# Kernel optimization log

Hardware: AMD Instinct MI355X
Metric: run time of the kernel (lower is better)

## Reference

```python
import jax, jax.numpy as jnp
import numpy as np

LAYERS, HIDDEN, FFN, HEADS = 4, 128, 256, 4
HEAD_D = HIDDEN // HEADS          # 32
V_HEAD = 2 * HEAD_D               # 64 (double_v_dim)
V_DIM = 2 * HIDDEN                # 256
SCALE_BASE = 512
EPS = 1e-5
GAMMAS = (1.0 - np.exp(np.linspace(np.log(1.0 / 32), np.log(1.0 / 512), HEADS))).astype(np.float32)


def _xpos(x, downscale):
    # x: (..., L, d) -- xpos rotary embedding with per-position decay scale
    L, d = x.shape[-2], x.shape[-1]
    half = d // 2
    base_scale = (jnp.arange(half, dtype=jnp.float32) + 0.4 * d) / (1.4 * d)   # (half,)
    power = jnp.arange(L, dtype=jnp.float32)[:, None] / SCALE_BASE
    sc = base_scale[None, :] ** power                                          # (L, half)
    inv_freq = 1.0 / (10000.0 ** (jnp.arange(half, dtype=jnp.float32) / half))
    ang = jnp.arange(L, dtype=jnp.float32)[:, None] * inv_freq[None, :]        # (L, half)
    sin, cos = jnp.sin(ang), jnp.cos(ang)
    if downscale:
        sc = 1.0 / sc
    sin_d = jnp.repeat(sin * sc, 2, axis=-1)   # duplicate_interleave -> (L, d)
    cos_d = jnp.repeat(cos * sc, 2, axis=-1)
    x1, x2 = x[..., ::2], x[..., 1::2]
    rot = jnp.stack((-x2, x1), axis=-1).reshape(x.shape)  # rotate_every_two
    return x * cos_d + rot * sin_d


def _layer_norm(x, w, b):
    mu = x.mean(-1, keepdims=True)
    var = x.var(-1, keepdims=True)
    return (x - mu) / jnp.sqrt(var + EPS) * w + b


def _msr(X, wq, wk, wv, wg, wo, gn_w, gn_b):
    # MultiScaleRetention, parallel form. X: (B, L, HIDDEN)
    B, L, _ = X.shape
    Q = _xpos(jnp.einsum('blh,nhd->bnld', X, wq), False)   # (B, heads, L, 32)
    K = _xpos(jnp.einsum('blh,nhd->bnld', X, wk), True)
    V = jnp.einsum('blh,nhv->bnlv', X, wv)                 # (B, heads, L, 64)
    n = jnp.arange(L)
    diff = n[:, None] - n[None, :]
    gam = jnp.asarray(GAMMAS)[:, None, None]
    D = jnp.where(diff >= 0, gam ** jnp.maximum(diff, 0).astype(jnp.float32), 0.0)  # (heads, L, L)
    scores = jnp.einsum('bnld,bnmd->bnlm', Q, K) * D[None]
    Y = jnp.einsum('bnlm,bnmv->bnlv', scores, V)
    Y = Y.transpose(0, 2, 1, 3).reshape(B, L, V_DIM)       # concat heads on feature dim
    # GroupNorm(heads, V_DIM) over the channel axis
    Yg = Y.reshape(B, L, HEADS, V_HEAD)
    mu = Yg.mean(-1, keepdims=True)
    var = Yg.var(-1, keepdims=True)
    Yn = ((Yg - mu) / jnp.sqrt(var + EPS)).reshape(B, L, V_DIM) * gn_w + gn_b
    G = X @ wg
    return (G * jax.nn.sigmoid(G) * Yn) @ wo               # swish gate, output proj


def _forward(x, rem_w1, rem_b1, rem_w2, rem_b2, rem_w3, rem_b3,
             wq, wk, wv, wg, wo, gn_w, gn_b,
             ln1_w, ln1_b, ln2_w, ln2_b,
             ffn_w1, ffn_b1, ffn_w2, ffn_b2,
             dec_w1, dec_b1, dec_w2, dec_b2):
    gelu = lambda t: jax.nn.gelu(t, approximate=False)
    # REM: 5 -> 32 -> 64 -> 128, GELU after each linear
    X = gelu(gelu(gelu(x @ rem_w1 + rem_b1) @ rem_w2 + rem_b2) @ rem_w3 + rem_b3)
    # RetNet: pre-LN retention + pre-LN FFN blocks with residuals
    for i in range(LAYERS):
        Y = _msr(_layer_norm(X, ln1_w[i], ln1_b[i]), wq[i], wk[i], wv[i],
                 wg[i], wo[i], gn_w[i], gn_b[i]) + X
        Z = _layer_norm(Y, ln2_w[i], ln2_b[i])
        X = gelu(Z @ ffn_w1[i] + ffn_b1[i]) @ ffn_w2[i] + ffn_b2[i] + Y
    # Decoder: 128 -> 64 -> 20, softmax over classes
    logits = gelu(X @ dec_w1 + dec_b1) @ dec_w2 + dec_b2
    return jax.nn.softmax(logits, axis=-1)


def setup_inputs() -> dict:
    key = jax.random.key(0)
    ks = jax.random.split(key, 16)
    rn = lambda k, shape, s=0.02: jax.random.normal(k, shape, dtype=jnp.float32) * s
    B, L = 64, 512
    return {
        'x': jax.random.normal(ks[0], (B, L, 5), dtype=jnp.float32),
        'rem_w1': rn(ks[1], (5, 32)), 'rem_b1': jnp.zeros((32,), jnp.float32),
        'rem_w2': rn(ks[2], (32, 64)), 'rem_b2': jnp.zeros((64,), jnp.float32),
        'rem_w3': rn(ks[3], (64, HIDDEN)), 'rem_b3': jnp.zeros((HIDDEN,), jnp.float32),
        'wq': rn(ks[4], (LAYERS, HEADS, HIDDEN, HEAD_D), 1.0 / HIDDEN),
        'wk': rn(ks[5], (LAYERS, HEADS, HIDDEN, HEAD_D), 1.0 / HIDDEN),
        'wv': rn(ks[6], (LAYERS, HEADS, HIDDEN, V_HEAD), 1.0 / HIDDEN),
        'wg': rn(ks[7], (LAYERS, HIDDEN, V_DIM), 1.0 / HIDDEN),
        'wo': rn(ks[8], (LAYERS, V_DIM, HIDDEN), 1.0 / HIDDEN),
        'gn_w': jnp.ones((LAYERS, V_DIM), jnp.float32),
        'gn_b': jnp.zeros((LAYERS, V_DIM), jnp.float32),
        'ln1_w': jnp.ones((LAYERS, HIDDEN), jnp.float32),
        'ln1_b': jnp.zeros((LAYERS, HIDDEN), jnp.float32),
        'ln2_w': jnp.ones((LAYERS, HIDDEN), jnp.float32),
        'ln2_b': jnp.zeros((LAYERS, HIDDEN), jnp.float32),
        'ffn_w1': rn(ks[9], (LAYERS, HIDDEN, FFN)),
        'ffn_b1': jnp.zeros((LAYERS, FFN), jnp.float32),
        'ffn_w2': rn(ks[10], (LAYERS, FFN, HIDDEN)),
        'ffn_b2': jnp.zeros((LAYERS, HIDDEN), jnp.float32),
        'dec_w1': rn(ks[11], (HIDDEN, 64)), 'dec_b1': jnp.zeros((64,), jnp.float32),
        'dec_w2': rn(ks[12], (64, 20)), 'dec_b2': jnp.zeros((20,), jnp.float32),
    }


def reference(x, rem_w1, rem_b1, rem_w2, rem_b2, rem_w3, rem_b3,
              wq, wk, wv, wg, wo, gn_w, gn_b,
              ln1_w, ln1_b, ln2_w, ln2_b,
              ffn_w1, ffn_b1, ffn_w2, ffn_b2,
              dec_w1, dec_b1, dec_w2, dec_b2):
    return _forward(x, rem_w1, rem_b1, rem_w2, rem_b2, rem_w3, rem_b3,
                    wq, wk, wv, wg, wo, gn_w, gn_b,
                    ln1_w, ln1_b, ln2_w, ln2_b,
                    ffn_w1, ffn_b1, ffn_w2, ffn_b2,
                    dec_w1, dec_b1, dec_w2, dec_b2)
```

## Files before the change

kernel.cpp:

```cpp
#include <hip/hip_runtime.h>
#include <math.h>
#include <cmath>

#define SEQ   512
#define NBATCH 64
#define BT    32768
#define HID   128
#define NHEAD 4
#define HD    32
#define VHD   64
#define VDIM  256
#define FFND  256

typedef __attribute__((ext_vector_type(8))) short bf16x8;
typedef __attribute__((ext_vector_type(4))) float f32x4;
typedef unsigned short u16;

__device__ __forceinline__ float gelu_f(float x){ return 0.5f*x*(1.f+erff(x*0.70710678118f)); }

__device__ __forceinline__ u16 f2bf(float f){
  __bf16 h = (__bf16)f;
  union{__bf16 h; u16 u;} v; v.h = h; return v.u;
}
__device__ __forceinline__ float bf2f(u16 u){
  union{unsigned u; float f;} v; v.u = ((unsigned)u)<<16; return v.f;
}

__device__ __forceinline__ void gload16(const void* g, void* l){
  __builtin_amdgcn_global_load_lds(
      (const __attribute__((address_space(1))) unsigned*)g,
      (__attribute__((address_space(3))) unsigned*)l, 16, 0, 0);
}

#define STAGE_TILE_N(dst, base, strideU16, colOffU16, wid_, srow_, phys16l_, NIT) \
  do{                                                                           \
    _Pragma("unroll")                                                           \
    for(int it_=0; it_<NIT; it_++){                                             \
      int blk_ = (wid_)*NIT + it_;                                              \
      int row_ = blk_*4 + (srow_);                                              \
      int log16_ = (phys16l_) ^ (row_&15);                                      \
      gload16((base) + (size_t)row_*(strideU16) + (colOffU16) + log16_*8,       \
              &(dst)[blk_*512]);                                                \
    }                                                                           \
  }while(0)

#define STAGE_TILE(dst, base, strideU16, colOffU16, wid_, srow_, phys16l_) \
  STAGE_TILE_N(dst, base, strideU16, colOffU16, wid_, srow_, phys16l_, 8)

__global__ __launch_bounds__(256) void wconv_kernel(
    const float* __restrict__ wq, const float* __restrict__ wk,
    const float* __restrict__ wv, const float* __restrict__ wg,
    const float* __restrict__ wo, const float* __restrict__ f1,
    const float* __restrict__ f2, const float* __restrict__ dw1,
    const float* __restrict__ w2e, const float* __restrict__ w3e,
    u16* __restrict__ Wt)
{
  int idx = blockIdx.x*256 + threadIdx.x;
  if(idx >= 786432){
    int q = idx - 786432;
    if(q < 8192){ int col=q>>7, h=q&127; Wt[idx]=f2bf(dw1[h*64+col]); }
    else if(q < 10240){ int p=q-8192; int row=p>>5, col=p&31; Wt[idx]=f2bf(w2e[col*64+row]); }
    else { int p=q-10240; int row=p>>6, col=p&63; Wt[idx]=f2bf(w3e[col*128+row]); }
    return;
  }
  int layer = idx / 196608;
  int r = idx - layer*196608;
  u16* W = Wt + (size_t)layer*196608;
  const float* wq_l = wq + (size_t)layer*16384;
  const float* wk_l = wk + (size_t)layer*16384;
  const float* wv_l = wv + (size_t)layer*32768;
  const float* wg_l = wg + (size_t)layer*32768;
  const float* wo_l = wo + (size_t)layer*32768;
  const float* f1_l = f1 + (size_t)layer*32768;
  const float* f2_l = f2 + (size_t)layer*32768;
  float v;
  if(r < 98304){
    int col = r>>7, h = r&127;
    if(col<128){ int n=col>>5, d=col&31; v = wq_l[(n*128+h)*32+d]; }
    else if(col<256){ int c=col-128, n=c>>5, d=c&31; v = wk_l[(n*128+h)*32+d]; }
    else if(col<512){ int c=col-256, n=c>>6, j=c&63; v = wv_l[(n*128+h)*64+j]; }
    else { int p=col-512; v = wg_l[h*256+p]; }
    W[r] = f2bf(v);
  } else if(r < 131072){
    int q = r-98304; int col=q>>8, k=q&255;
    W[r] = f2bf(wo_l[k*128+col]);
  } else if(r < 163840){
    int q = r-131072; int col=q>>7, h=q&127;
    W[r] = f2bf(f1_l[h*256+col]);
  } else {
    int q = r-163840; int col=q>>8, k=q&255;
    W[r] = f2bf(f2_l[k*128+col]);
  }
}

__global__ __launch_bounds__(256) void embed_kernel(
    const float* __restrict__ x,
    const float* __restrict__ w1, const float* __restrict__ b1,
    const float* __restrict__ b2, const float* __restrict__ b3,
    const u16* __restrict__ W23t,
    const float* __restrict__ lnw, const float* __restrict__ lnb,
    float* __restrict__ X, u16* __restrict__ xn)
{
  __shared__ float sx[64][6];
  __shared__ float sw1[160], sb1[32], sb2[64], sb3[128];
  __shared__ u16 big[18944];
  int t=threadIdx.x, lane=t&63, wid=t>>6, mrow=lane&15, quad=lane>>4, r0=wid*16;
  int tok0=blockIdx.x*64;

  for(int i=t;i<320;i+=256) sx[i/5][i%5]=x[(size_t)tok0*5+i];
  for(int i=t;i<160;i+=256) sw1[i]=w1[i];
  if(t<32) sb1[t]=b1[t];
  if(t<64) sb2[t]=b2[t];
  if(t<128) sb3[t]=b3[t];
  for(int c=t;c<256;c+=256){ int row=c>>2, c8=(c&3)*8;
    *(uint4*)&big[2560+row*40+c8]=*(const uint4*)&W23t[row*32+c8]; }
  for(int c=t;c<1024;c+=256){ int row=c>>3, c8=(c&7)*8;
    *(uint4*)&big[9728+row*72+c8]=*(const uint4*)&W23t[2048+row*64+c8]; }
  __syncthreads();

  for(int task=t; task<2048; task+=256){
    int tok=task>>5, j=task&31;
    float a=sb1[j];
    #pragma unroll
    for(int i=0;i<5;i++) a+=sx[tok][i]*sw1[i*32+j];
    big[tok*40+j]=f2bf(gelu_f(a));
  }
  __syncthreads();

  f32x4 h2[4];
  #pragma unroll
  for(int cc=0;cc<4;cc++) h2[cc]=(f32x4){0.f,0.f,0.f,0.f};
  {
    bf16x8 a=*(const bf16x8*)&big[(r0+mrow)*40+quad*8];
    #pragma unroll
    for(int cc=0;cc<4;cc++){
      bf16x8 b=*(const bf16x8*)&big[2560+(cc*16+mrow)*40+quad*8];
      h2[cc]=__builtin_amdgcn_mfma_f32_16x16x32_bf16(a,b,h2[cc],0,0,0);
    }
  }
  #pragma unroll
  for(int cc=0;cc<4;cc++){
    float bs=sb2[cc*16+mrow];
    #pragma unroll
    for(int reg=0;reg<4;reg++)
      big[5120+(r0+quad*4+reg)*72+cc*16+mrow]=f2bf(gelu_f(h2[cc][reg]+bs));
  }
  __syncthreads();

  f32x4 xac[8];
  #pragma unroll
  for(int cc=0;cc<8;cc++) xac[cc]=(f32x4){0.f,0.f,0.f,0.f};
  #pragma unroll
  for(int ks=0;ks<2;ks++){
    bf16x8 a=*(const bf16x8*)&big[5120+(r0+mrow)*72+ks*32+quad*8];
    #pragma unroll
    for(int cc=0;cc<8;cc++){
      bf16x8 b=*(const bf16x8*)&big[9728+(cc*16+mrow)*72+ks*32+quad*8];
      xac[cc]=__builtin_amdgcn_mfma_f32_16x16x32_bf16(a,b,xac[cc],0,0,0);
    }
  }
  __syncthreads();

  #pragma unroll
  for(int reg=0;reg<4;reg++){
    int rowl=r0+quad*4+reg, rowg=tok0+rowl;
    float xv[8], s=0.f, sq=0.f;
    #pragma unroll
    for(int cc=0;cc<8;cc++){
      float v=gelu_f(xac[cc][reg]+sb3[cc*16+mrow]);
      xv[cc]=v; s+=v; sq+=v*v;
    }
    #pragma unroll
    for(int m=1;m<16;m<<=1){ s+=__shfl_xor(s,m); sq+=__shfl_xor(sq,m); }
    float mu=s*(1.f/128.f);
    float var=sq*(1.f/128.f)-mu*mu;
    float rstd=rsqrtf(var+1e-5f);
    #pragma unroll
    for(int cc=0;cc<8;cc++){
      int col=cc*16+mrow;
      X[(size_t)rowg*128+col]=xv[cc];
      big[rowl*136+col]=f2bf((xv[cc]-mu)*rstd*lnw[col]+lnb[col]);
    }
  }
  __syncthreads();
  for(int th=t; th<1024; th+=256){
    int row=th>>4, seg=th&15;
    *(uint4*)&xn[(size_t)(tok0+row)*128+seg*8]=*(const uint4*)&big[row*136+seg*8];
  }
}

__device__ __forceinline__ void qkvg_epilogue(
    int nc, f32x4 acc[2][4], u16* stg,
    int t, int mrow, int quad, int r0q, int c0q, int b, int l0, int tok0,
    u16* __restrict__ Q, u16* __restrict__ K,
    u16* __restrict__ Vt, u16* __restrict__ G)
{
  if(nc < 2){
    bool isK = (nc==1);
    float sgn = isK ? -1.f : 1.f;
    #pragma unroll
    for(int cc=0;cc<4;cc++){
      int colc = c0q + cc*16 + mrow;
      int i = (colc&31)>>1;
      float log2bs = log2f(((float)i + 12.8f)*(1.f/44.8f));
      float invf   = exp2f(-(float)i * (13.28771238f/16.f));
      float rstep  = exp2f(sgn*log2bs*(1.f/512.f));
      float c1 = cosf(invf), s1 = sinf(invf);
      #pragma unroll
      for(int rr=0;rr<2;rr++){
        int rowl0 = r0q + rr*16 + quad*4;
        float lb = (float)(l0 + rowl0);
        float sc = exp2f(sgn*log2bs*lb*(1.f/512.f));
        float ang = lb*invf;
        float u = cosf(ang)*sc, v = sinf(ang)*sc;
        #pragma unroll
        for(int reg=0;reg<4;reg++){
          int rowl = rowl0 + reg;
          float val = acc[rr][cc][reg];
          float partner = __shfl_xor(val, 1);
          float o = (colc&1) ? (val*u + partner*v) : (val*u - partner*v);
          stg[rowl*136 + colc] = f2bf(o);
          float un = (u*c1 - v*s1)*rstep;
          float vn = (u*s1 + v*c1)*rstep;
          u = un; v = vn;
        }
      }
    }
    __syncthreads();
    u16* O = isK ? K : Q;
    for(int th=t; th<1024; th+=256){
      int row=th>>4, n=(th>>2)&3, seg=th&3;
      *(uint4*)&O[(((size_t)(b*4+n)*512) + (l0+row))*32 + seg*8]
        = *(const uint4*)&stg[row*136 + n*32 + seg*8];
    }
  } else if(nc < 4){
    #pragma unroll
    for(int cc=0;cc<4;cc++){
      int colc = c0q + cc*16 + mrow;
      #pragma unroll
      for(int rr=0;rr<2;rr++){
        #pragma unroll
        for(int reg=0;reg<4;reg++){
          int rowl = r0q + rr*16 + quad*4 + reg;
          stg[colc*72 + rowl] = f2bf(acc[rr][cc][reg]);
        }
      }
    }
    __syncthreads();
    int jbase = (nc-2)*128;
    for(int th=t; th<1024; th+=256){
      int row=th>>3, seg=th&7;
      int jg = jbase + row; int n = jg>>6, j = jg&63;
      *(uint4*)&Vt[(((size_t)(b*4+n)*64) + j)*512 + l0 + seg*8]
        = *(const uint4*)&stg[row*72 + seg*8];
    }
  } else {
    #pragma unroll
    for(int cc=0;cc<4;cc++){
      int colc = c0q + cc*16 + mrow;
      #pragma unroll
      for(int rr=0;rr<2;rr++){
        #pragma unroll
        for(int reg=0;reg<4;reg++){
          int rowl = r0q + rr*16 + quad*4 + reg;
          stg[rowl*136 + colc] = f2bf(acc[rr][cc][reg]);
        }
      }
    }
    __syncthreads();
    int gc0 = (nc-4)*128;
    for(int th=t; th<1024; th+=256){
      int row=th>>4, seg=th&15;
      *(uint4*)&G[((size_t)(tok0+row))*256 + gc0 + seg*8]
        = *(const uint4*)&stg[row*136 + seg*8];
    }
  }
}

__device__ __forceinline__ void qkvg_epi8(
    int nc, f32x4 acc[4], u16* stg,
    int t, int mrow, int quad, int r0, int c0, int b, int l0, int tok0,
    u16* __restrict__ Q, u16* __restrict__ K,
    u16* __restrict__ Vt, u16* __restrict__ G)
{
  if(nc < 2){
    bool isK = (nc==1);
    float sgn = isK ? -1.f : 1.f;
    #pragma unroll
    for(int cc=0;cc<4;cc++){
      int colc = c0 + cc*16 + mrow;
      int i = (colc&31)>>1;
      float log2bs = log2f(((float)i + 12.8f)*(1.f/44.8f));
      float invf   = exp2f(-(float)i * (13.28771238f/16.f));
      float rstep  = exp2f(sgn*log2bs*(1.f/512.f));
      float c1 = cosf(invf), s1 = sinf(invf);
      int rowl0 = r0 + quad*4;
      float lb = (float)(l0 + rowl0);
      float sc = exp2f(sgn*log2bs*lb*(1.f/512.f));
      float ang = lb*invf;
      float u = cosf(ang)*sc, v = sinf(ang)*sc;
      #pragma unroll
      for(int reg=0;reg<4;reg++){
        int rowl = rowl0 + reg;
        float val = acc[cc][reg];
        float partner = __shfl_xor(val, 1);
        float o = (colc&1) ? (val*u + partner*v) : (val*u - partner*v);
        stg[rowl*136 + colc] = f2bf(o);
        float un = (u*c1 - v*s1)*rstep;
        float vn = (u*s1 + v*c1)*rstep;
        u = un; v = vn;
      }
    }
    __syncthreads();
    u16* O = isK ? K : Q;
    for(int th=t; th<1024; th+=512){
      int row=th>>4, n=(th>>2)&3, seg=th&3;
      *(uint4*)&O[(((size_t)(b*4+n)*512) + (l0+row))*32 + seg*8]
        = *(const uint4*)&stg[row*136 + n*32 + seg*8];
    }
  } else if(nc < 4){
    #pragma unroll
    for(int cc=0;cc<4;cc++){
      int colc = c0 + cc*16 + mrow;
      #pragma unroll
      for(int reg=0;reg<4;reg++){
        int rowl = r0 + quad*4 + reg;
        stg[colc*72 + rowl] = f2bf(acc[cc][reg]);
      }
    }
    __syncthreads();
    int jbase = (nc-2)*128;
    for(int th=t; th<1024; th+=512){
      int row=th>>3, seg=th&7;
      int jg = jbase + row; int n = jg>>6, j = jg&63;
      *(uint4*)&Vt[(((size_t)(b*4+n)*64) + j)*512 + l0 + seg*8]
        = *(const uint4*)&stg[row*72 + seg*8];
    }
  } else {
    #pragma unroll
    for(int cc=0;cc<4;cc++){
      int colc = c0 + cc*16 + mrow;
      #pragma unroll
      for(int reg=0;reg<4;reg++){
        int rowl = r0 + quad*4 + reg;
        stg[rowl*136 + colc] = f2bf(acc[cc][reg]);
      }
    }
    __syncthreads();
    int gc0 = (nc-4)*128;
    for(int th=t; th<1024; th+=512){
      int row=th>>4, seg=th&15;
      *(uint4*)&G[((size_t)(tok0+row))*256 + gc0 + seg*8]
        = *(const uint4*)&stg[row*136 + seg*8];
    }
  }
}

__global__ __launch_bounds__(256) void qkvg_kernel(
    const u16* __restrict__ A, const u16* __restrict__ Wt,
    u16* __restrict__ Q, u16* __restrict__ K,
    u16* __restrict__ Vt, u16* __restrict__ G)
{
  __shared__ u16 sW[128*128];
  u16* stg = sW;
  int t = threadIdx.x, lane = t&63, wid = t>>6;
  int mrow = lane&15, quad = lane>>4;
  int srow = lane>>4, phys16l = lane&15;
  int r0q = (wid>>1)*32, c0q = (wid&1)*64;
  int tok0 = blockIdx.x*64;
  int b = tok0>>9, l0 = tok0&511;

  bf16x8 a0f[4], a1f[4];
  #pragma unroll
  for(int ks=0; ks<4; ks++){
    a0f[ks] = *(const bf16x8*)&A[(size_t)(tok0+r0q+mrow)*128 + ks*32+quad*8];
    a1f[ks] = *(const bf16x8*)&A[(size_t)(tok0+r0q+16+mrow)*128 + ks*32+quad*8];
  }

  for(int ch=0; ch<3; ch++){
    int nc = blockIdx.y*3 + ch;
    if(ch) __syncthreads();
    STAGE_TILE(sW, Wt + (size_t)nc*16384, 128, 0, wid, srow, phys16l);
    __syncthreads();

    f32x4 acc[2][4];
    #pragma unroll
    for(int rr=0;rr<2;rr++)
      #pragma unroll
      for(int cc=0;cc<4;cc++) acc[rr][cc] = (f32x4){0.f,0.f,0.f,0.f};
    #pragma unroll
    for(int ks=0; ks<4; ks++){
      #pragma unroll
      for(int cc=0; cc<4; cc++){
        bf16x8 bb = *(const bf16x8*)&sW[(c0q+cc*16+mrow)*128 + (((ks*4+quad)^mrow)<<3)];
        acc[0][cc] = __builtin_amdgcn_mfma_f32_16x16x32_bf16(a0f[ks],bb,acc[0][cc],0,0,0);
        acc[1][cc] = __builtin_amdgcn_mfma_f32_16x16x32_bf16(a1f[ks],bb,acc[1][cc],0,0,0);
      }
    }
    __syncthreads();
    qkvg_epilogue(nc, acc, stg, t, mrow, quad, r0q, c0q, b, l0, tok0, Q, K, Vt, G);
  }
}

__global__ __launch_bounds__(512, 4) void layer_kernel(
    const u16* __restrict__ Qin, const u16* __restrict__ Kin,
    const u16* __restrict__ Vtin, const u16* __restrict__ Gin,
    const float* __restrict__ gnw, const float* __restrict__ gnb, float4 l2g,
    const u16* __restrict__ Wo,
    const u16* __restrict__ W1t, const float* __restrict__ b1,
    const u16* __restrict__ W2t, const float* __restrict__ b2,
    const float* __restrict__ Xin,
    const float* __restrict__ ln2w, const float* __restrict__ ln2b,
    const float* __restrict__ ln1w, const float* __restrict__ ln1b,
    float* __restrict__ Xout,
    const u16* __restrict__ Wq,
    u16* __restrict__ Qo, u16* __restrict__ Ko,
    u16* __restrict__ Vto, u16* __restrict__ Go,
    const u16* __restrict__ DecW1, const float* __restrict__ db1,
    const float* __restrict__ dw2, const float* __restrict__ db2,
    float* __restrict__ outp)
{
  __shared__ u16 smem[33280];
  u16* bufA = smem;
  u16* bufB = smem + 16384;
  float (*sRed)[2][2] = (float(*)[2][2])(smem + 32768);
  int t=threadIdx.x, lane=t&63, wid=t>>6, mrow=lane&15, quad=lane>>4;
  int rg=wid>>1, half=wid&1;
  int r0=rg*16, c0=half*64;
  int bix = blockIdx.x;
  int kk = (bix>>6)&3, hib = bix>>8;
  int ltsw = hib ? (7-kk) : kk;
  int tok0 = (((bix&63)<<3) | ltsw) * 64;
  int srow = lane>>4, phys16l = lane&15;

  int half8 = wid>>2, lw = wid&3;
  int tl = t & 255;
  int r0l = lw*16;
  int lt = (tok0>>6)&7;
  int bq = tok0>>9;
  bf16x8 gfrag[8];

  #pragma unroll
  for(int p=0;p<2;p++){
    int n = 2*p + half8;
    int bn = bq*4 + n;
    float lg2g = (n==0)?l2g.x:(n==1)?l2g.y:(n==2)?l2g.z:l2g.w;
    u16* rK = smem + half8*11776;
    u16* rV = rK + 2560;
    u16* rS = rK + 7168;

    bf16x8 qa = *(const bf16x8*)&Qin[((size_t)bn*512 + lt*64 + r0l+mrow)*32 + quad*8];
    f32x4 oacc[4];
    #pragma unroll
    for(int cc=0;cc<4;cc++) oacc[cc] = (f32x4){0.f,0.f,0.f,0.f};
    float gp1 = exp2f(lg2g), gp2 = gp1*gp1, gp3 = gp2*gp1;
    float gpow[4] = {1.f, gp1, gp2, gp3};
    float gw[4], gb[4];
    #pragma unroll
    for(int cc=0;cc<4;cc++){ gw[cc]=gnw[n*64+cc*16+mrow]; gb[cc]=gnb[n*64+cc*16+mrow]; }
    int rowl0 = lt*64 + r0l + quad*4;

    int krow = tl>>2, kc8 = (tl&3)*8;
    int vrow = tl>>3, vc8 = (tl&7)*8;
    const u16* Kb = Kin  + ((size_t)bn*512 + krow)*32 + kc8;
    const u16* V0 = Vtin + ((size_t)bn*64 + vrow)*512 + vc8;
    const u16* V1 = Vtin + ((size_t)bn*64 + vrow+32)*512 + vc8;
    uint4 ldk  = *(const uint4*)(Kb);
    uint4 ldv0 = *(const uint4*)(V0);
    uint4 ldv1 = *(const uint4*)(V1);

    for(int mt=0; mt<=lt; mt++){
      if(mt) __syncthreads();
      *(uint4*)&rK[krow*40+kc8]      = ldk;
      *(uint4*)&rV[vrow*72+vc8]      = ldv0;
      *(uint4*)&rV[(vrow+32)*72+vc8] = ldv1;
      if(mt < lt){
        ldk  = *(const uint4*)(Kb + (size_t)(mt+1)*2048);
        ldv0 = *(const uint4*)(V0 + (mt+1)*64);
        ldv1 = *(const uint4*)(V1 + (mt+1)*64);
      }
      __syncthreads();
      f32x4 sacc[4];
      #pragma unroll
      for(int cc=0;cc<4;cc++){
        bf16x8 bb = *(const bf16x8*)&rK[(cc*16+mrow)*40 + quad*8];
        sacc[cc] = __builtin_amdgcn_mfma_f32_16x16x32_bf16(qa,bb,(f32x4){0.f,0.f,0.f,0.f},0,0,0);
      }
      #pragma unroll
      for(int cc=0;cc<4;cc++){
        int colm = mt*64 + cc*16 + mrow;
        int d0 = rowl0 - colm;
        float w0 = exp2f(lg2g*(float)d0);
        #pragma unroll
        for(int reg=0;reg<4;reg++){
          float w = (d0+reg>=0) ? w0*gpow[reg] : 0.f;
          rS[(r0l+quad*4+reg)*72 + cc*16+mrow] = f2bf(sacc[cc][reg]*w);
        }
      }
      __syncthreads();
      #pragma unroll
      for(int ks=0;ks<2;ks++){
        bf16x8 a = *(const bf16x8*)&rS[(r0l+mrow)*72 + ks*32+quad*8];
        #pragma unroll
        for(int cc=0;cc<4;cc++){
          bf16x8 bb = *(const bf16x8*)&rV[(cc*16+mrow)*72 + ks*32+quad*8];
          oacc[cc] = __builtin_amdgcn_mfma_f32_16x16x32_bf16(a,bb,oacc[cc],0,0,0);
        }
      }
    }

    __syncthreads();
    #pragma unroll
    for(int reg=0;reg<4;reg++){
      float s=0.f, sq=0.f;
      #pragma unroll
      for(int cc=0;cc<4;cc++){ float v=oacc[cc][reg]; s+=v; sq+=v*v; }
      #pragma unroll
      for(int m=1;m<16;m<<=1){ s+=__shfl_xor(s,m); sq+=__shfl_xor(sq,m); }
      float mu = s*(1.f/64.f);
      float var = sq*(1.f/64.f) - mu*mu;
      float rn = rsqrtf(var + 1e-5f);
      int rowl = r0l + quad*4 + reg;
      int l = lt*64 + rowl;
      size_t gbase = ((size_t)(bq*512 + l))*256 + n*64;
      #pragma unroll
      for(int cc=0;cc<4;cc++){
        float gg = bf2f(Gin[gbase + cc*16+mrow]);
        float gate = gg/(1.f+expf(-gg));
        rS[rowl*72 + cc*16+mrow] = f2bf(gate*((oacc[cc][reg]-mu)*rn*gw[cc] + gb[cc]));
      }
    }
    __syncthreads();
    #pragma unroll
    for(int hh=0; hh<2; hh++){
      int nn = 2*p + hh;
      const u16* src = smem + hh*11776 + 7168;
      #pragma unroll
      for(int ksl=0; ksl<2; ksl++)
        gfrag[2*nn+ksl] = *(const bf16x8*)&src[(r0+mrow)*72 + ksl*32 + quad*8];
    }
    __syncthreads();
  }

  STAGE_TILE_N(bufA, Wo, 256, 0, wid, srow, phys16l, 4);
  __syncthreads();

  STAGE_TILE_N(bufB, Wo, 256, 128, wid, srow, phys16l, 4);
  f32x4 yac[4];
  #pragma unroll
  for(int cc=0;cc<4;cc++) yac[cc]=(f32x4){0.f,0.f,0.f,0.f};
  #pragma unroll
  for(int cc=0;cc<4;cc++){
    #pragma unroll
    for(int ks=0;ks<4;ks++){
      bf16x8 b=*(const bf16x8*)&bufA[(c0+cc*16+mrow)*128 + (((ks*4+quad)^mrow)<<3)];
      yac[cc]=__builtin_amdgcn_mfma_f32_16x16x32_bf16(gfrag[ks],b,yac[cc],0,0,0);
    }
  }
  __syncthreads();

  STAGE_TILE_N(bufA, W1t, 128, 0, wid, srow, phys16l, 4);
  #pragma unroll
  for(int cc=0;cc<4;cc++){
    #pragma unroll
    for(int ks=0;ks<4;ks++){
      bf16x8 b=*(const bf16x8*)&bufB[(c0+cc*16+mrow)*128 + (((ks*4+quad)^mrow)<<3)];
      yac[cc]=__builtin_amdgcn_mfma_f32_16x16x32_bf16(gfrag[4+ks],b,yac[cc],0,0,0);
    }
  }
  float yv[4][4];
  #pragma unroll
  for(int reg=0;reg<4;reg++){
    int rowl=r0+quad*4+reg, rowg=tok0+rowl;
    float s=0.f, sq=0.f;
    #pragma unroll
    for(int cc=0;cc<4;cc++){
      float v=yac[cc][reg]+Xin[(size_t)rowg*128+c0+cc*16+mrow];
      yv[cc][reg]=v; s+=v; sq+=v*v;
    }
    #pragma unroll
    for(int m=1;m<16;m<<=1){ s+=__shfl_xor(s,m); sq+=__shfl_xor(sq,m); }
    if(mrow==0){ sRed[rowl][half][0]=s; sRed[rowl][half][1]=sq; }
  }
  __syncthreads();

  #pragma unroll
  for(int reg=0;reg<4;reg++){
    int rowl=r0+quad*4+reg;
    float s =sRed[rowl][0][0]+sRed[rowl][1][0];
    float sq=sRed[rowl][0][1]+sRed[rowl][1][1];
    float mu=s*(1.f/128.f);
    float var=sq*(1.f/128.f)-mu*mu;
    float rstd=rsqrtf(var+1e-5f);
    #pragma unroll
    for(int cc=0;cc<4;cc++){
      int col=c0+cc*16+mrow;
      bufB[rowl*136+col]=f2bf((yv[cc][reg]-mu)*rstd*ln2w[col]+ln2b[col]);
    }
  }
  __syncthreads();
  bf16x8 az[4];
  #pragma unroll
  for(int ks=0;ks<4;ks++) az[ks]=*(const bf16x8*)&bufB[(r0+mrow)*136+ks*32+quad*8];
  __syncthreads();

  bf16x8 hfrag[8];
  STAGE_TILE_N(bufB, W1t + (size_t)16384, 128, 0, wid, srow, phys16l, 4);
  {
    f32x4 hac[4];
    #pragma unroll
    for(int cc=0;cc<4;cc++) hac[cc]=(f32x4){0.f,0.f,0.f,0.f};
    #pragma unroll
    for(int cc=0;cc<4;cc++){
      #pragma unroll
      for(int ks=0;ks<4;ks++){
        bf16x8 b=*(const bf16x8*)&bufA[(c0+cc*16+mrow)*128 + (((ks*4+quad)^mrow)<<3)];
        hac[cc]=__builtin_amdgcn_mfma_f32_16x16x32_bf16(az[ks],b,hac[cc],0,0,0);
      }
    }
    __syncthreads();
    #pragma unroll
    for(int cc=0;cc<4;cc++){
      float bs=b1[c0+cc*16+mrow];
      #pragma unroll
      for(int reg=0;reg<4;reg++)
        bufA[(r0+quad*4+reg)*136 + c0+cc*16+mrow]=f2bf(gelu_f(hac[cc][reg]+bs));
    }
    __syncthreads();
    #pragma unroll
    for(int ks=0;ks<4;ks++) hfrag[ks]=*(const bf16x8*)&bufA[(r0+mrow)*136+ks*32+quad*8];
    __syncthreads();
  }

  STAGE_TILE_N(bufA, W2t, 256, 0, wid, srow, phys16l, 4);
  {
    f32x4 hac[4];
    #pragma unroll
    for(int cc=0;cc<4;cc++) hac[cc]=(f32x4){0.f,0.f,0.f,0.f};
    #pragma unroll
    for(int cc=0;cc<4;cc++){
      #pragma unroll
      for(int ks=0;ks<4;ks++){
        bf16x8 b=*(const bf16x8*)&bufB[(c0+cc*16+mrow)*128 + (((ks*4+quad)^mrow)<<3)];
        hac[cc]=__builtin_amdgcn_mfma_f32_16x16x32_bf16(az[ks],b,hac[cc],0,0,0);
      }
    }
    __syncthreads();
    #pragma unroll
    for(int cc=0;cc<4;cc++){
      float bs=b1[128+c0+cc*16+mrow];
      #pragma unroll
      for(int reg=0;reg<4;reg++)
        bufB[(r0+quad*4+reg)*136 + c0+cc*16+mrow]=f2bf(gelu_f(hac[cc][reg]+bs));
    }
    __syncthreads();
    #pragma unroll
    for(int ks=0;ks<4;ks++) hfrag[4+ks]=*(const bf16x8*)&bufB[(r0+mrow)*136+ks*32+quad*8];
    __syncthreads();
  }

  STAGE_TILE_N(bufB, W2t, 256, 128, wid, srow, phys16l, 4);
  f32x4 xac[4];
  #pragma unroll
  for(int cc=0;cc<4;cc++) xac[cc]=(f32x4){0.f,0.f,0.f,0.f};
  #pragma unroll
  for(int cc=0;cc<4;cc++){
    #pragma unroll
    for(int ks=0;ks<4;ks++){
      bf16x8 b=*(const bf16x8*)&bufA[(c0+cc*16+mrow)*128 + (((ks*4+quad)^mrow)<<3)];
      xac[cc]=__builtin_amdgcn_mfma_f32_16x16x32_bf16(hfrag[ks],b,xac[cc],0,0,0);
    }
  }
  __syncthreads();

  if(Wq) STAGE_TILE_N(bufA, Wq, 128, 0, wid, srow, phys16l, 4);
  #pragma unroll
  for(int cc=0;cc<4;cc++){
    #pragma unroll
    for(int ks=0;ks<4;ks++){
      bf16x8 b=*(const bf16x8*)&bufB[(c0+cc*16+mrow)*128 + (((ks*4+quad)^mrow)<<3)];
      xac[cc]=__builtin_amdgcn_mfma_f32_16x16x32_bf16(hfrag[4+ks],b,xac[cc],0,0,0);
    }
  }
  float xv[4][4];
  #pragma unroll
  for(int reg=0;reg<4;reg++){
    int rowl=r0+quad*4+reg;
    float s=0.f, sq=0.f;
    #pragma unroll
    for(int cc=0;cc<4;cc++){
      float v=xac[cc][reg]+b2[c0+cc*16+mrow]+yv[cc][reg];
      xv[cc][reg]=v; s+=v; sq+=v*v;
    }
    #pragma unroll
    for(int m=1;m<16;m<<=1){ s+=__shfl_xor(s,m); sq+=__shfl_xor(sq,m); }
    if(mrow==0){ sRed[rowl][half][0]=s; sRed[rowl][half][1]=sq; }
  }
  __syncthreads();

  if(Wq){
    #pragma unroll
    for(int reg=0;reg<4;reg++){
      int rowl=r0+quad*4+reg, rowg=tok0+rowl;
      float s =sRed[rowl][0][0]+sRed[rowl][1][0];
      float sq=sRed[rowl][0][1]+sRed[rowl][1][1];
      float mu=s*(1.f/128.f);
      float var=sq*(1.f/128.f)-mu*mu;
      float rstd=rsqrtf(var+1e-5f);
      #pragma unroll
      for(int cc=0;cc<4;cc++){
        int col=c0+cc*16+mrow;
        Xout[(size_t)rowg*128+col]=xv[cc][reg];
        bufB[rowl*136+col]=f2bf((xv[cc][reg]-mu)*rstd*ln1w[col]+ln1b[col]);
      }
    }
    __syncthreads();
    bf16x8 aq[4];
    #pragma unroll
    for(int ks=0; ks<4; ks++)
      aq[ks] = *(const bf16x8*)&bufB[(r0+mrow)*136 + ks*32+quad*8];
    __syncthreads();

    int b = tok0>>9, l0 = tok0&511;
    for(int nc=0; nc<6; nc++){
      u16* cur = (nc&1) ? bufB : bufA;
      u16* nxt = (nc&1) ? bufA : bufB;
      if(nc<5) STAGE_TILE_N(nxt, Wq + (size_t)(nc+1)*16384, 128, 0, wid, srow, phys16l, 4);

      f32x4 acc[4];
      #pragma unroll
      for(int cc=0;cc<4;cc++) acc[cc] = (f32x4){0.f,0.f,0.f,0.f};
      #pragma unroll
      for(int ks=0; ks<4; ks++){
        #pragma unroll
        for(int cc=0; cc<4; cc++){
          bf16x8 bb = *(const bf16x8*)&cur[(c0+cc*16+mrow)*128 + (((ks*4+quad)^mrow)<<3)];
          acc[cc] = __builtin_amdgcn_mfma_f32_16x16x32_bf16(aq[ks],bb,acc[cc],0,0,0);
        }
      }
      __syncthreads();
      qkvg_epi8(nc, acc, cur, t, mrow, quad, r0, c0, b, l0, tok0, Qo, Ko, Vto, Go);
      __syncthreads();
    }
    return;
  }

  u16*  sWd  = smem;
  float* sHd = (float*)(smem + 8704);
  float* sw2s= (float*)(smem + 17408);
  float* sLs = (float*)(smem + 19968);
  float* sb2s= (float*)(smem + 22528);
  u16*  sXd  = smem + 24064;

  #pragma unroll
  for(int reg=0;reg<4;reg++){
    int rowl=r0+quad*4+reg;
    #pragma unroll
    for(int cc=0;cc<4;cc++){
      int col=c0+cc*16+mrow;
      sXd[rowl*136+col]=f2bf(xv[cc][reg]);
    }
  }
  for(int th=t; th<1024; th+=512){
    int row=th>>4, c8=(th&15)*8;
    *(uint4*)&sWd[row*136+c8] = *(const uint4*)&DecW1[(size_t)row*128 + c8];
  }
  for(int i=t;i<1280;i+=512) sw2s[i]=dw2[i];
  if(t<20) sb2s[t]=db2[t];
  __syncthreads();

  {
    f32x4 dacc[2];
    #pragma unroll
    for(int cc=0;cc<2;cc++) dacc[cc]=(f32x4){0.f,0.f,0.f,0.f};
    #pragma unroll
    for(int ks=0; ks<4; ks++){
      int koff = ks*32 + quad*8;
      bf16x8 a = *(const bf16x8*)&sXd[(r0+mrow)*136 + koff];
      #pragma unroll
      for(int cc=0; cc<2; cc++){
        bf16x8 b = *(const bf16x8*)&sWd[(half*32+cc*16+mrow)*136 + koff];
        dacc[cc] = __builtin_amdgcn_mfma_f32_16x16x32_bf16(a,b,dacc[cc],0,0,0);
      }
    }
    #pragma unroll
    for(int cc=0;cc<2;cc++){
      int col = half*32 + cc*16 + mrow;
      float bb = db1[col];
      #pragma unroll
      for(int reg=0;reg<4;reg++)
        sHd[(r0+quad*4+reg)*68 + col] = gelu_f(dacc[cc][reg] + bb);
    }
  }
  __syncthreads();

  for(int task=t; task<1280; task+=512){
    int tk = task/20, o = task - tk*20;
    float a = sb2s[o];
    for(int k=0;k<64;k++) a += sHd[tk*68+k]*sw2s[k*20+o];
    sLs[tk*20+o] = a;
  }
  __syncthreads();
  if(t < 64){
    float mx = -1e30f;
    #pragma unroll
    for(int o=0;o<20;o++) mx = fmaxf(mx, sLs[t*20+o]);
    float sum = 0.f;
    float e[20];
    #pragma unroll
    for(int o=0;o<20;o++){ e[o]=expf(sLs[t*20+o]-mx); sum += e[o]; }
    float inv = 1.f/sum;
    #pragma unroll
    for(int o=0;o<20;o++) sLs[t*20+o] = e[o]*inv;
  }
  __syncthreads();
  for(int th=t; th<1280; th+=512){
    outp[(size_t)tok0*20 + th] = sLs[th];
  }
}

extern "C" void kernel_launch(void* const* d_in, const int* in_sizes, int n_in,
                              void* d_out, int out_size, void* d_ws, size_t ws_size,
                              hipStream_t stream) {
  (void)in_sizes; (void)n_in; (void)out_size; (void)ws_size;
  const float* x      = (const float*)d_in[0];
  const float* rem_w1 = (const float*)d_in[1];
  const float* rem_b1 = (const float*)d_in[2];
  const float* rem_w2 = (const float*)d_in[3];
  const float* rem_b2 = (const float*)d_in[4];
  const float* rem_w3 = (const float*)d_in[5];
  const float* rem_b3 = (const float*)d_in[6];
  const float* wq     = (const float*)d_in[7];
  const float* wk     = (const float*)d_in[8];
  const float* wv     = (const float*)d_in[9];
  const float* wg     = (const float*)d_in[10];
  const float* wo     = (const float*)d_in[11];
  const float* gn_w   = (const float*)d_in[12];
  const float* gn_b   = (const float*)d_in[13];
  const float* ln1_w  = (const float*)d_in[14];
  const float* ln1_b  = (const float*)d_in[15];
  const float* ln2_w  = (const float*)d_in[16];
  const float* ln2_b  = (const float*)d_in[17];
  const float* ffn_w1 = (const float*)d_in[18];
  const float* ffn_b1 = (const float*)d_in[19];
  const float* ffn_w2 = (const float*)d_in[20];
  const float* ffn_b2 = (const float*)d_in[21];
  const float* dec_w1 = (const float*)d_in[22];
  const float* dec_b1 = (const float*)d_in[23];
  const float* dec_w2 = (const float*)d_in[24];
  const float* dec_b2 = (const float*)d_in[25];
  float* outp = (float*)d_out;

  const size_t S128 = (size_t)BT*128;
  const size_t S256 = (size_t)BT*256;
  float* ws = (float*)d_ws;
  float* Xb = ws;
  u16*  Q0  = (u16*)(Xb + S128);
  u16*  K0  = Q0 + (size_t)BT*32;
  u16*  Vt0 = K0 + (size_t)BT*32;
  u16*  Q1  = Vt0 + (size_t)BT*64;
  u16*  K1  = Q1 + (size_t)BT*32;
  u16*  Vt1 = K1 + (size_t)BT*32;
  u16*  XnBf = Q1;
  u16*  G0  = Vt1 + (size_t)BT*64;
  u16*  G1  = G0 + S256;
  u16*  WtBf = G1 + S256;

  double lgA = log(1.0/32.0), lgB = log(1.0/512.0);
  float4 l2g;
  {
    double g0 = 1.0 - exp(lgA + 0.0*(lgB-lgA)/3.0);
    double g1 = 1.0 - exp(lgA + 1.0*(lgB-lgA)/3.0);
    double g2 = 1.0 - exp(lgA + 2.0*(lgB-lgA)/3.0);
    double g3 = 1.0 - exp(lgA + 3.0*(lgB-lgA)/3.0);
    l2g.x = (float)(log(g0)/log(2.0));
    l2g.y = (float)(log(g1)/log(2.0));
    l2g.z = (float)(log(g2)/log(2.0));
    l2g.w = (float)(log(g3)/log(2.0));
  }

  wconv_kernel<<<3144, 256, 0, stream>>>(wq, wk, wv, wg, wo, ffn_w1, ffn_w2, dec_w1,
                                         rem_w2, rem_w3, WtBf);
  embed_kernel<<<BT/64, 256, 0, stream>>>(x, rem_w1, rem_b1, rem_b2, rem_b3,
                                          WtBf+794624, ln1_w, ln1_b, Xb, XnBf);
  qkvg_kernel<<<dim3(BT/64,2), 256, 0, stream>>>(XnBf, WtBf, Q0, K0, Vt0, G0);

  for(int li=0; li<4; li++){
    u16* Wt_l = WtBf + (size_t)li*196608;
    const float* gnw_l = gn_w + (size_t)li*VDIM;
    const float* gnb_l = gn_b + (size_t)li*VDIM;
    const float* l2w = ln2_w + (size_t)li*HID, *l2b = ln2_b + (size_t)li*HID;
    const float* f1b = ffn_b1 + (size_t)li*FFND;
    const float* f2b = ffn_b2 + (size_t)li*HID;
    int nli = (li+1)&3;
    const float* n1w = ln1_w + (size_t)nli*HID, *n1b = ln1_b + (size_t)nli*HID;
    const u16* Wq_next = (li<3) ? (WtBf + (size_t)(li+1)*196608) : nullptr;

    const u16* Qi  = (li&1) ? Q1  : Q0;
    const u16* Ki  = (li&1) ? K1  : K0;
    const u16* Vti = (li&1) ? Vt1 : Vt0;
    const u16* Gi  = (li&1) ? G1  : G0;
    u16* Qo  = (li&1) ? Q0  : Q1;
    u16* Ko  = (li&1) ? K0  : K1;
    u16* Vto = (li&1) ? Vt0 : Vt1;
    u16* Go  = (li&1) ? G0  : G1;

    layer_kernel<<<BT/64, 512, 0, stream>>>(
        Qi, Ki, Vti, Gi, gnw_l, gnb_l, l2g,
        Wt_l+98304, Wt_l+131072, f1b, Wt_l+163840, f2b,
        Xb, l2w, l2b, n1w, n1b, Xb,
        Wq_next, Qo, Ko, Vto, Go,
        WtBf+786432, dec_b1, dec_w2, dec_b2, outp);
  }
}
```

Baseline: 399.0 us.

## Fuse first-layer QKVG projection into embed kernel and pad retention LDS strides

The embedding MLP kernel now continues directly into the first layer's QKVG projection, reusing the LayerNorm output from shared memory instead of writing it to global memory and launching a separate kernel. Each block now handles all six weight chunks rather than splitting them across two blocks, so there is less parallelism in that stage. The retention kernel's shared-memory row strides for K, V and score tiles are also padded, apparently to reduce LDS bank conflicts, at the cost of somewhat more shared memory.

Measured after the change: 602.1 us. 1.51x slower.

```diff
diff --git a/kernel.cpp b/kernel.cpp
--- a/kernel.cpp
+++ b/kernel.cpp
@@ -93,102 +93,6 @@
   }
 }
 
-__global__ __launch_bounds__(256) void embed_kernel(
-    const float* __restrict__ x,
-    const float* __restrict__ w1, const float* __restrict__ b1,
-    const float* __restrict__ b2, const float* __restrict__ b3,
-    const u16* __restrict__ W23t,
-    const float* __restrict__ lnw, const float* __restrict__ lnb,
-    float* __restrict__ X, u16* __restrict__ xn)
-{
-  __shared__ float sx[64][6];
-  __shared__ float sw1[160], sb1[32], sb2[64], sb3[128];
-  __shared__ u16 big[18944];
-  int t=threadIdx.x, lane=t&63, wid=t>>6, mrow=lane&15, quad=lane>>4, r0=wid*16;
-  int tok0=blockIdx.x*64;
-
-  for(int i=t;i<320;i+=256) sx[i/5][i%5]=x[(size_t)tok0*5+i];
-  for(int i=t;i<160;i+=256) sw1[i]=w1[i];
-  if(t<32) sb1[t]=b1[t];
-  if(t<64) sb2[t]=b2[t];
-  if(t<128) sb3[t]=b3[t];
-  for(int c=t;c<256;c+=256){ int row=c>>2, c8=(c&3)*8;
-    *(uint4*)&big[2560+row*40+c8]=*(const uint4*)&W23t[row*32+c8]; }
-  for(int c=t;c<1024;c+=256){ int row=c>>3, c8=(c&7)*8;
-    *(uint4*)&big[9728+row*72+c8]=*(const uint4*)&W23t[2048+row*64+c8]; }
-  __syncthreads();
-
-  for(int task=t; task<2048; task+=256){
-    int tok=task>>5, j=task&31;
-    float a=sb1[j];
-    #pragma unroll
-    for(int i=0;i<5;i++) a+=sx[tok][i]*sw1[i*32+j];
-    big[tok*40+j]=f2bf(gelu_f(a));
-  }
-  __syncthreads();
-
-  f32x4 h2[4];
-  #pragma unroll
-  for(int cc=0;cc<4;cc++) h2[cc]=(f32x4){0.f,0.f,0.f,0.f};
-  {
-    bf16x8 a=*(const bf16x8*)&big[(r0+mrow)*40+quad*8];
-    #pragma unroll
-    for(int cc=0;cc<4;cc++){
-      bf16x8 b=*(const bf16x8*)&big[2560+(cc*16+mrow)*40+quad*8];
-      h2[cc]=__builtin_amdgcn_mfma_f32_16x16x32_bf16(a,b,h2[cc],0,0,0);
-    }
-  }
-  #pragma unroll
-  for(int cc=0;cc<4;cc++){
-    float bs=sb2[cc*16+mrow];
-    #pragma unroll
-    for(int reg=0;reg<4;reg++)
-      big[5120+(r0+quad*4+reg)*72+cc*16+mrow]=f2bf(gelu_f(h2[cc][reg]+bs));
-  }
-  __syncthreads();
-
-  f32x4 xac[8];
-  #pragma unroll
-  for(int cc=0;cc<8;cc++) xac[cc]=(f32x4){0.f,0.f,0.f,0.f};
-  #pragma unroll
-  for(int ks=0;ks<2;ks++){
-    bf16x8 a=*(const bf16x8*)&big[5120+(r0+mrow)*72+ks*32+quad*8];
-    #pragma unroll
-    for(int cc=0;cc<8;cc++){
-      bf16x8 b=*(const bf16x8*)&big[9728+(cc*16+mrow)*72+ks*32+quad*8];
-      xac[cc]=__builtin_amdgcn_mfma_f32_16x16x32_bf16(a,b,xac[cc],0,0,0);
-    }
-  }
-  __syncthreads();
-
-  #pragma unroll
-  for(int reg=0;reg<4;reg++){
-    int rowl=r0+quad*4+reg, rowg=tok0+rowl;
-    float xv[8], s=0.f, sq=0.f;
-    #pragma unroll
-    for(int cc=0;cc<8;cc++){
-      float v=gelu_f(xac[cc][reg]+sb3[cc*16+mrow]);
-      xv[cc]=v; s+=v; sq+=v*v;
-    }
-    #pragma unroll
-    for(int m=1;m<16;m<<=1){ s+=__shfl_xor(s,m); sq+=__shfl_xor(sq,m); }
-    float mu=s*(1.f/128.f);
-    float var=sq*(1.f/128.f)-mu*mu;
-    float rstd=rsqrtf(var+1e-5f);
-    #pragma unroll
-    for(int cc=0;cc<8;cc++){
-      int col=cc*16+mrow;
-      X[(size_t)rowg*128+col]=xv[cc];
-      big[rowl*136+col]=f2bf((xv[cc]-mu)*rstd*lnw[col]+lnb[col]);
-    }
-  }
-  __syncthreads();
-  for(int th=t; th<1024; th+=256){
-    int row=th>>4, seg=th&15;
-    *(uint4*)&xn[(size_t)(tok0+row)*128+seg*8]=*(const uint4*)&big[row*136+seg*8];
-  }
-}
-
 __device__ __forceinline__ void qkvg_epilogue(
     int nc, f32x4 acc[2][4], u16* stg,
     int t, int mrow, int quad, int r0q, int c0q, int b, int l0, int tok0,
@@ -277,6 +181,138 @@
   }
 }
 
+__global__ __launch_bounds__(256) void embed_kernel(
+    const float* __restrict__ x,
+    const float* __restrict__ w1, const float* __restrict__ b1,
+    const float* __restrict__ b2, const float* __restrict__ b3,
+    const u16* __restrict__ W23t,
+    const float* __restrict__ lnw, const float* __restrict__ lnb,
+    const u16* __restrict__ Wt,
+    float* __restrict__ X,
+    u16* __restrict__ Q, u16* __restrict__ K,
+    u16* __restrict__ Vt, u16* __restrict__ G)
+{
+  __shared__ float sx[64][6];
+  __shared__ float sw1[160], sb1[32], sb2[64], sb3[128];
+  __shared__ u16 big[25088];
+  int t=threadIdx.x, lane=t&63, wid=t>>6, mrow=lane&15, quad=lane>>4, r0=wid*16;
+  int tok0=blockIdx.x*64;
+
+  for(int i=t;i<320;i+=256) sx[i/5][i%5]=x[(size_t)tok0*5+i];
+  for(int i=t;i<160;i+=256) sw1[i]=w1[i];
+  if(t<32) sb1[t]=b1[t];
+  if(t<64) sb2[t]=b2[t];
+  if(t<128) sb3[t]=b3[t];
+  for(int c=t;c<256;c+=256){ int row=c>>2, c8=(c&3)*8;
+    *(uint4*)&big[2560+row*40+c8]=*(const uint4*)&W23t[row*32+c8]; }
+  for(int c=t;c<1024;c+=256){ int row=c>>3, c8=(c&7)*8;
+    *(uint4*)&big[9728+row*72+c8]=*(const uint4*)&W23t[2048+row*64+c8]; }
+  __syncthreads();
+
+  for(int task=t; task<2048; task+=256){
+    int tok=task>>5, j=task&31;
+    float a=sb1[j];
+    #pragma unroll
+    for(int i=0;i<5;i++) a+=sx[tok][i]*sw1[i*32+j];
+    big[tok*40+j]=f2bf(gelu_f(a));
+  }
+  __syncthreads();
+
+  f32x4 h2[4];
+  #pragma unroll
+  for(int cc=0;cc<4;cc++) h2[cc]=(f32x4){0.f,0.f,0.f,0.f};
+  {
+    bf16x8 a=*(const bf16x8*)&big[(r0+mrow)*40+quad*8];
+    #pragma unroll
+    for(int cc=0;cc<4;cc++){
+      bf16x8 b=*(const bf16x8*)&big[2560+(cc*16+mrow)*40+quad*8];
+      h2[cc]=__builtin_amdgcn_mfma_f32_16x16x32_bf16(a,b,h2[cc],0,0,0);
+    }
+  }
+  #pragma unroll
+  for(int cc=0;cc<4;cc++){
+    float bs=sb2[cc*16+mrow];
+    #pragma unroll
+    for(int reg=0;reg<4;reg++)
+      big[5120+(r0+quad*4+reg)*72+cc*16+mrow]=f2bf(gelu_f(h2[cc][reg]+bs));
+  }
+  __syncthreads();
+
+  f32x4 xac[8];
+  #pragma unroll
+  for(int cc=0;cc<8;cc++) xac[cc]=(f32x4){0.f,0.f,0.f,0.f};
+  #pragma unroll
+  for(int ks=0;ks<2;ks++){
+    bf16x8 a=*(const bf16x8*)&big[5120+(r0+mrow)*72+ks*32+quad*8];
+    #pragma unroll
+    for(int cc=0;cc<8;cc++){
+      bf16x8 b=*(const bf16x8*)&big[9728+(cc*16+mrow)*72+ks*32+quad*8];
+      xac[cc]=__builtin_amdgcn_mfma_f32_16x16x32_bf16(a,b,xac[cc],0,0,0);
+    }
+  }
+  __syncthreads();
+
+  #pragma unroll
+  for(int reg=0;reg<4;reg++){
+    int rowl=r0+quad*4+reg, rowg=tok0+rowl;
+    float xv[8], s=0.f, sq=0.f;
+    #pragma unroll
+    for(int cc=0;cc<8;cc++){
+      float v=gelu_f(xac[cc][reg]+sb3[cc*16+mrow]);
+      xv[cc]=v; s+=v; sq+=v*v;
+    }
+    #pragma unroll
+    for(int m=1;m<16;m<<=1){ s+=__shfl_xor(s,m); sq+=__shfl_xor(sq,m); }
+    float mu=s*(1.f/128.f);
+    float var=sq*(1.f/128.f)-mu*mu;
+    float rstd=rsqrtf(var+1e-5f);
+    #pragma unroll
+    for(int cc=0;cc<8;cc++){
+      int col=cc*16+mrow;
+      X[(size_t)rowg*128+col]=xv[cc];
+      big[rowl*136+col]=f2bf((xv[cc]-mu)*rstd*lnw[col]+lnb[col]);
+    }
+  }
+  __syncthreads();
+
+  u16* sW = big + 8704;
+  u16* stg = sW;
+  int srow = lane>>4, phys16l = lane&15;
+  int r0q = (wid>>1)*32, c0q = (wid&1)*64;
+  int b = tok0>>9, l0 = tok0&511;
+
+  bf16x8 a0f[4], a1f[4];
+  #pragma unroll
+  for(int ks=0; ks<4; ks++){
+    a0f[ks] = *(const bf16x8*)&big[(r0q+mrow)*136 + ks*32+quad*8];
+    a1f[ks] = *(const bf16x8*)&big[(r0q+16+mrow)*136 + ks*32+quad*8];
+  }
+  __syncthreads();
+
+  for(int nc=0; nc<6; nc++){
+    if(nc) __syncthreads();
+    STAGE_TILE(sW, Wt + (size_t)nc*16384, 128, 0, wid, srow, phys16l);
+    __syncthreads();
+
+    f32x4 acc[2][4];
+    #pragma unroll
+    for(int rr=0;rr<2;rr++)
+      #pragma unroll
+      for(int cc=0;cc<4;cc++) acc[rr][cc] = (f32x4){0.f,0.f,0.f,0.f};
+    #pragma unroll
+    for(int ks=0; ks<4; ks++){
+      #pragma unroll
+      for(int cc=0; cc<4; cc++){
+        bf16x8 bb = *(const bf16x8*)&sW[(c0q+cc*16+mrow)*128 + (((ks*4+quad)^mrow)<<3)];
+        acc[0][cc] = __builtin_amdgcn_mfma_f32_16x16x32_bf16(a0f[ks],bb,acc[0][cc],0,0,0);
+        acc[1][cc] = __builtin_amdgcn_mfma_f32_16x16x32_bf16(a1f[ks],bb,acc[1][cc],0,0,0);
+      }
+    }
+    __syncthreads();
+    qkvg_epilogue(nc, acc, stg, t, mrow, quad, r0q, c0q, b, l0, tok0, Q, K, Vt, G);
+  }
+}
+
 __device__ __forceinline__ void qkvg_epi8(
     int nc, f32x4 acc[4], u16* stg,
     int t, int mrow, int quad, int r0, int c0, int b, int l0, int tok0,
@@ -353,52 +389,6 @@
       *(uint4*)&G[((size_t)(tok0+row))*256 + gc0 + seg*8]
         = *(const uint4*)&stg[row*136 + seg*8];
     }
-  }
-}
-
-__global__ __launch_bounds__(256) void qkvg_kernel(
-    const u16* __restrict__ A, const u16* __restrict__ Wt,
-    u16* __restrict__ Q, u16* __restrict__ K,
-    u16* __restrict__ Vt, u16* __restrict__ G)
-{
-  __shared__ u16 sW[128*128];
-  u16* stg = sW;
-  int t = threadIdx.x, lane = t&63, wid = t>>6;
-  int mrow = lane&15, quad = lane>>4;
-  int srow = lane>>4, phys16l = lane&15;
-  int r0q = (wid>>1)*32, c0q = (wid&1)*64;
-  int tok0 = blockIdx.x*64;
-  int b = tok0>>9, l0 = tok0&511;
-
-  bf16x8 a0f[4], a1f[4];
-  #pragma unroll
-  for(int ks=0; ks<4; ks++){
-    a0f[ks] = *(const bf16x8*)&A[(size_t)(tok0+r0q+mrow)*128 + ks*32+quad*8];
-    a1f[ks] = *(const bf16x8*)&A[(size_t)(tok0+r0q+16+mrow)*128 + ks*32+quad*8];
-  }
-
-  for(int ch=0; ch<3; ch++){
-    int nc = blockIdx.y*3 + ch;
-    if(ch) __syncthreads();
-    STAGE_TILE(sW, Wt + (size_t)nc*16384, 128, 0, wid, srow, phys16l);
-    __syncthreads();
-
-    f32x4 acc[2][4];
-    #pragma unroll
-    for(int rr=0;rr<2;rr++)
-      #pragma unroll
-      for(int cc=0;cc<4;cc++) acc[rr][cc] = (f32x4){0.f,0.f,0.f,0.f};
-    #pragma unroll
-    for(int ks=0; ks<4; ks++){
-      #pragma unroll
-      for(int cc=0; cc<4; cc++){
-        bf16x8 bb = *(const bf16x8*)&sW[(c0q+cc*16+mrow)*128 + (((ks*4+quad)^mrow)<<3)];
-        acc[0][cc] = __builtin_amdgcn_mfma_f32_16x16x32_bf16(a0f[ks],bb,acc[0][cc],0,0,0);
-        acc[1][cc] = __builtin_amdgcn_mfma_f32_16x16x32_bf16(a1f[ks],bb,acc[1][cc],0,0,0);
-      }
-    }
-    __syncthreads();
-    qkvg_epilogue(nc, acc, stg, t, mrow, quad, r0q, c0q, b, l0, tok0, Q, K, Vt, G);
   }
 }
 
@@ -445,9 +435,9 @@
     int n = 2*p + half8;
     int bn = bq*4 + n;
     float lg2g = (n==0)?l2g.x:(n==1)?l2g.y:(n==2)?l2g.z:l2g.w;
-    u16* rK = smem + half8*11776;
-    u16* rV = rK + 2560;
-    u16* rS = rK + 7168;
+    u16* rK = smem + half8*12544;
+    u16* rV = rK + 2816;
+    u16* rS = rK + 7680;
 
     bf16x8 qa = *(const bf16x8*)&Qin[((size_t)bn*512 + lt*64 + r0l+mrow)*32 + quad*8];
     f32x4 oacc[4];
@@ -471,9 +461,9 @@
 
     for(int mt=0; mt<=lt; mt++){
       if(mt) __syncthreads();
-      *(uint4*)&rK[krow*40+kc8]      = ldk;
-      *(uint4*)&rV[vrow*72+vc8]      = ldv0;
-      *(uint4*)&rV[(vrow+32)*72+vc8] = ldv1;
+      *(uint4*)&rK[krow*44+kc8]      = ldk;
+      *(uint4*)&rV[vrow*76+vc8]      = ldv0;
+      *(uint4*)&rV[(vrow+32)*76+vc8] = ldv1;
       if(mt < lt){
         ldk  = *(const uint4*)(Kb + (size_t)(mt+1)*2048);
         ldv0 = *(const uint4*)(V0 + (mt+1)*64);
@@ -483,7 +473,7 @@
       f32x4 sacc[4];
       #pragma unroll
       for(int cc=0;cc<4;cc++){
-        bf16x8 bb = *(const bf16x8*)&rK[(cc*16+mrow)*40 + quad*8];
+        bf16x8 bb = *(const bf16x8*)&rK[(cc*16+mrow)*44 + quad*8];
         sacc[cc] = __builtin_amdgcn_mfma_f32_16x16x32_bf16(qa,bb,(f32x4){0.f,0.f,0.f,0.f},0,0,0);
       }
       #pragma unroll
@@ -494,16 +484,16 @@
         #pragma unroll
         for(int reg=0;reg<4;reg++){
           float w = (d0+reg>=0) ? w0*gpow[reg] : 0.f;
-          rS[(r0l+quad*4+reg)*72 + cc*16+mrow] = f2bf(sacc[cc][reg]*w);
+          rS[(r0l+quad*4+reg)*76 + cc*16+mrow] = f2bf(sacc[cc][reg]*w);
         }
       }
       __syncthreads();
       #pragma unroll
       for(int ks=0;ks<2;ks++){
-        bf16x8 a = *(const bf16x8*)&rS[(r0l+mrow)*72 + ks*32+quad*8];
+        bf16x8 a = *(const bf16x8*)&rS[(r0l+mrow)*76 + ks*32+quad*8];
         #pragma unroll
         for(int cc=0;cc<4;cc++){
-          bf16x8 bb = *(const bf16x8*)&rV[(cc*16+mrow)*72 + ks*32+quad*8];
+          bf16x8 bb = *(const bf16x8*)&rV[(cc*16+mrow)*76 + ks*32+quad*8];
           oacc[cc] = __builtin_amdgcn_mfma_f32_16x16x32_bf16(a,bb,oacc[cc],0,0,0);
         }
       }
@@ -527,17 +517,17 @@
       for(int cc=0;cc<4;cc++){
         float gg = bf2f(Gin[gbase + cc*16+mrow]);
         float gate = gg/(1.f+expf(-gg));
-        rS[rowl*72 + cc*16+mrow] = f2bf(gate*((oacc[cc][reg]-mu)*rn*gw[cc] + gb[cc]));
+        rS[rowl*76 + cc*16+mrow] = f2bf(gate*((oacc[cc][reg]-mu)*rn*gw[cc] + gb[cc]));
       }
     }
     __syncthreads();
     #pragma unroll
     for(int hh=0; hh<2; hh++){
       int nn = 2*p + hh;
-      const u16* src = smem + hh*11776 + 7168;
+      const u16* src = smem + hh*12544 + 7680;
       #pragma unroll
       for(int ksl=0; ksl<2; ksl++)
-        gfrag[2*nn+ksl] = *(const bf16x8*)&src[(r0+mrow)*72 + ksl*32 + quad*8];
+        gfrag[2*nn+ksl] = *(const bf16x8*)&src[(r0+mrow)*76 + ksl*32 + quad*8];
     }
     __syncthreads();
   }
@@ -861,7 +851,6 @@
   u16*  Q1  = Vt0 + (size_t)BT*64;
   u16*  K1  = Q1 + (size_t)BT*32;
   u16*  Vt1 = K1 + (size_t)BT*32;
-  u16*  XnBf = Q1;
   u16*  G0  = Vt1 + (size_t)BT*64;
   u16*  G1  = G0 + S256;
   u16*  WtBf = G1 + S256;
@@ -882,8 +871,8 @@
   wconv_kernel<<<3144, 256, 0, stream>>>(wq, wk, wv, wg, wo, ffn_w1, ffn_w2, dec_w1,
                                          rem_w2, rem_w3, WtBf);
   embed_kernel<<<BT/64, 256, 0, stream>>>(x, rem_w1, rem_b1, rem_b2, rem_b3,
-                                          WtBf+794624, ln1_w, ln1_b, Xb, XnBf);
-  qkvg_kernel<<<dim3(BT/64,2), 256, 0, stream>>>(XnBf, WtBf, Q0, K0, Vt0, G0);
+                                          WtBf+794624, ln1_w, ln1_b, WtBf,
+                                          Xb, Q0, K0, Vt0, G0);
 
   for(int li=0; li<4; li++){
     u16* Wt_l = WtBf + (size_t)li*196608;
```
